# Kernel tuning notes

Hardware: AMD Instinct MI355X
Metric: run time of the kernel (lower is better)

The kernel has to match this reference:

```python
import jax, jax.numpy as jnp
import numpy as np

N_NODES = 100000
N_EDGES = 3200000
IN_CH, HID_CH, OUT_CH = 128, 64, 40


def gcn_conv(x, row, col, norm, W, b, n_nodes):
    # linear transform first (PyG GCNConv order), then normalized aggregation
    h = x @ W                                   # [N, out]
    msg = h[row] * norm[:, None]                # [E+N, out] gathered & scaled
    out = jax.ops.segment_sum(msg, col, num_segments=n_nodes)
    return out + b


def setup_inputs() -> dict:
    key = jax.random.key(0)
    k0, k1, k2, k3, k4, k5 = jax.random.split(key, 6)
    x = jax.random.normal(k0, (N_NODES, IN_CH), dtype=jnp.float32)
    edge_index = jax.random.randint(k1, (2, N_EDGES), 0, N_NODES, dtype=jnp.int64)
    # Glorot-ish init for weights
    W1 = jax.random.normal(k2, (IN_CH, HID_CH), dtype=jnp.float32) * (1.0 / np.sqrt(IN_CH))
    b1 = jnp.zeros((HID_CH,), dtype=jnp.float32)
    W2 = jax.random.normal(k3, (HID_CH, OUT_CH), dtype=jnp.float32) * (1.0 / np.sqrt(HID_CH))
    b2 = jnp.zeros((OUT_CH,), dtype=jnp.float32)
    return {"x": x, "edge_index": edge_index, "original_size": N_NODES,
            "W1": W1, "b1": b1, "W2": W2, "b2": b2}


def reference(x, edge_index, original_size, W1, b1, W2, b2):
    n = x.shape[0]
    # add self-loops (GCNConv default)
    loops = jnp.arange(n, dtype=edge_index.dtype)
    row = jnp.concatenate([edge_index[0], loops])   # source
    col = jnp.concatenate([edge_index[1], loops])   # target
    # symmetric normalization: deg over targets with unit edge weights
    deg = jax.ops.segment_sum(jnp.ones_like(col, dtype=x.dtype), col, num_segments=n)
    dinv = jnp.where(deg > 0, jax.lax.rsqrt(deg), 0.0)
    norm = dinv[row] * dinv[col]                    # [E+N]
    h = gcn_conv(x, row, col, norm, W1, b1, n)
    h = gcn_conv(h, row, col, norm, W2, b2, n)
    out = jax.nn.log_softmax(h, axis=1)
    return out[:original_size]
```

## Files before the change

### kernel.cpp

```cpp
#include <hip/hip_runtime.h>
#include <math.h>


#define NN 100000
#define NE 3200000
#define NBUK 391
#define BCAP 8704
#define EPB 16384


__global__ void k_zero(int* __restrict__ p, int n) {
  int i = blockIdx.x * blockDim.x + threadIdx.x;
  if (i < n) p[i] = 0;
}


__device__ __forceinline__ unsigned bf16rne(float x) {
  unsigned u = __float_as_uint(x);
  return (u + 0x7fffu + ((u >> 16) & 1u)) >> 16;
}
__device__ __forceinline__ unsigned pack2(float lo, float hi) {
  return bf16rne(lo) | (bf16rne(hi) << 16);
}


__global__ __launch_bounds__(256) void k_bucket(const int* __restrict__ ei,
                                                int* __restrict__ tail,
                                                unsigned* __restrict__ bucket) {
  __shared__ int hist[NBUK], wbase[NBUK], loc[NBUK];
  const int tid = threadIdx.x;
  const int beg = blockIdx.x * EPB;
  const int end = min(beg + EPB, NE);
  const int* col = ei + NE;
  for (int b = tid; b < NBUK; b += 256) { hist[b] = 0; loc[b] = 0; }
  __syncthreads();
  for (int e = beg + tid * 4; e < end; e += 1024) {
    int4 c4 = *(const int4*)(col + e);
    atomicAdd(&hist[c4.x >> 8], 1);
    atomicAdd(&hist[c4.y >> 8], 1);
    atomicAdd(&hist[c4.z >> 8], 1);
    atomicAdd(&hist[c4.w >> 8], 1);
  }
  __syncthreads();
  for (int b = tid; b < NBUK; b += 256)
    wbase[b] = atomicAdd(&tail[b], hist[b]);
  __syncthreads();
  for (int e = beg + tid * 4; e < end; e += 1024) {
    int4 c4 = *(const int4*)(col + e);
    int4 r4 = *(const int4*)(ei + e);
    {
      int b = c4.x >> 8;
      unsigned pos = (unsigned)(wbase[b] + atomicAdd(&loc[b], 1));
      if (pos < BCAP) bucket[(size_t)b * BCAP + pos] = ((unsigned)r4.x << 8) | (unsigned)(c4.x & 255);
    }
    {
      int b = c4.y >> 8;
      unsigned pos = (unsigned)(wbase[b] + atomicAdd(&loc[b], 1));
      if (pos < BCAP) bucket[(size_t)b * BCAP + pos] = ((unsigned)r4.y << 8) | (unsigned)(c4.y & 255);
    }
    {
      int b = c4.z >> 8;
      unsigned pos = (unsigned)(wbase[b] + atomicAdd(&loc[b], 1));
      if (pos < BCAP) bucket[(size_t)b * BCAP + pos] = ((unsigned)r4.z << 8) | (unsigned)(c4.z & 255);
    }
    {
      int b = c4.w >> 8;
      unsigned pos = (unsigned)(wbase[b] + atomicAdd(&loc[b], 1));
      if (pos < BCAP) bucket[(size_t)b * BCAP + pos] = ((unsigned)r4.w << 8) | (unsigned)(c4.w & 255);
    }
  }
}


__global__ void k_bstart(const int* __restrict__ tail, int* __restrict__ bstart) {
  const int tid = threadIdx.x, lane = tid & 63, wid = tid >> 6;
  int v = (tid < NBUK) ? min(tail[tid], BCAP) : 0;
  int s = v;
  #pragma unroll
  for (int d = 1; d < 64; d <<= 1) { int t = __shfl_up(s, d, 64); if (lane >= d) s += t; }
  __shared__ int wsum[8];
  if (lane == 63) wsum[wid] = s;
  __syncthreads();
  int wpre = 0;
  for (int w = 0; w < wid; ++w) wpre += wsum[w];
  int excl = wpre + s - v;
  if (tid <= NBUK) bstart[tid] = excl;
}


__global__ __launch_bounds__(256) void k_sort(const unsigned* __restrict__ bucket,
                                              const int* __restrict__ tail,
                                              const int* __restrict__ bstart,
                                              int* __restrict__ csr_src,
                                              int* __restrict__ offsets,
                                              float* __restrict__ dinv) {
  __shared__ int h[256], base_[256], loc[256];
  __shared__ int sorted[BCAP];
  __shared__ int wsum[4];
  const int b = blockIdx.x;
  const int lo = b << 8;
  const int nc = min(256, NN - lo);
  const int n = min(tail[b], BCAP);
  const int seg0 = bstart[b];
  const unsigned* __restrict__ bk = bucket + (size_t)b * BCAP;
  const int tid = threadIdx.x, lane = tid & 63, wid = tid >> 6;
  h[tid] = 0; loc[tid] = 0;
  __syncthreads();
  int i = tid * 4;
  for (; i + 3 < n; i += 1024) {
    uint4 v = *(const uint4*)(bk + i);
    atomicAdd(&h[v.x & 255u], 1);
    atomicAdd(&h[v.y & 255u], 1);
    atomicAdd(&h[v.z & 255u], 1);
    atomicAdd(&h[v.w & 255u], 1);
  }
  for (; i < n; ++i) atomicAdd(&h[bk[i] & 255u], 1);
  __syncthreads();
  {
    int v = h[tid];
    int s = v;
    #pragma unroll
    for (int d = 1; d < 64; d <<= 1) { int t = __shfl_up(s, d, 64); if (lane >= d) s += t; }
    if (lane == 63) wsum[wid] = s;
    __syncthreads();
    int wpre = 0;
    #pragma unroll
    for (int w = 0; w < 4; ++w) if (w < wid) wpre += wsum[w];
    int excl = wpre + s - v;
    base_[tid] = excl;
    if (tid < nc) {
      dinv[lo + tid] = rsqrtf((float)(v + 1));
      offsets[lo + tid] = seg0 + excl;
    }
  }
  if (b == 0 && tid == 0) offsets[NN] = bstart[NBUK];
  __syncthreads();
  i = tid * 4;
  for (; i + 3 < n; i += 1024) {
    uint4 v = *(const uint4*)(bk + i);
    { int c = v.x & 255u; sorted[base_[c] + atomicAdd(&loc[c], 1)] = (int)(v.x >> 8); }
    { int c = v.y & 255u; sorted[base_[c] + atomicAdd(&loc[c], 1)] = (int)(v.y >> 8); }
    { int c = v.z & 255u; sorted[base_[c] + atomicAdd(&loc[c], 1)] = (int)(v.z >> 8); }
    { int c = v.w & 255u; sorted[base_[c] + atomicAdd(&loc[c], 1)] = (int)(v.w >> 8); }
  }
  for (; i < n; ++i) {
    unsigned ent = bk[i];
    int c = ent & 255u;
    sorted[base_[c] + atomicAdd(&loc[c], 1)] = (int)(ent >> 8);
  }
  __syncthreads();
  for (int t = tid; t < n; t += 256) csr_src[seg0 + t] = sorted[t];
}


__global__ __launch_bounds__(256) void k_gemm1(const float* __restrict__ x,
                                               const float* __restrict__ W1,
                                               const float* __restrict__ dinv,
                                               unsigned* __restrict__ m1b) {
  __shared__ float ws[128 * 64];
  __shared__ float xt[16 * 132];
  const int tid = threadIdx.x;
  const int row0 = blockIdx.x * 128;
  {
    const float4* __restrict__ w4 = (const float4*)W1;
    float4* __restrict__ s4 = (float4*)ws;
    for (int i = tid; i < 128 * 16; i += 256) s4[i] = w4[i];
  }
  const int cg = tid & 7;
  const int rg = tid >> 3;
  const int srow = tid & 127;
  const int skh = tid >> 7;
  float acc[4][8];
  #pragma unroll
  for (int i = 0; i < 4; ++i)
    #pragma unroll
    for (int j = 0; j < 8; ++j) acc[i][j] = 0.f;
  const float4* __restrict__ xt4 = (const float4*)xt;
  const float4* __restrict__ ws4 = (const float4*)ws;
  for (int ks = 0; ks < 8; ++ks) {
    __syncthreads();
    {
      int grow = row0 + srow; if (grow > NN - 1) grow = NN - 1;
      const float* xp = x + (size_t)grow * 128 + ks * 16 + skh * 8;
      float4 va = *(const float4*)xp;
      float4 vb = *(const float4*)(xp + 4);
      const int kb = skh * 8;
      xt[(kb + 0) * 132 + srow] = va.x;
      xt[(kb + 1) * 132 + srow] = va.y;
      xt[(kb + 2) * 132 + srow] = va.z;
      xt[(kb + 3) * 132 + srow] = va.w;
      xt[(kb + 4) * 132 + srow] = vb.x;
      xt[(kb + 5) * 132 + srow] = vb.y;
      xt[(kb + 6) * 132 + srow] = vb.z;
      xt[(kb + 7) * 132 + srow] = vb.w;
    }
    __syncthreads();
    #pragma unroll 4
    for (int kk = 0; kk < 16; ++kk) {
      const int k = ks * 16 + kk;
      float4 xv = xt4[kk * 33 + rg];
      float4 wa = ws4[k * 16 + cg * 2];
      float4 wb = ws4[k * 16 + cg * 2 + 1];
      float xr[4] = {xv.x, xv.y, xv.z, xv.w};
      float wc[8] = {wa.x, wa.y, wa.z, wa.w, wb.x, wb.y, wb.z, wb.w};
      #pragma unroll
      for (int i = 0; i < 4; ++i)
        #pragma unroll
        for (int j = 0; j < 8; ++j)
          acc[i][j] = fmaf(xr[i], wc[j], acc[i][j]);
    }
  }
  #pragma unroll
  for (int i = 0; i < 4; ++i) {
    const int row = row0 + rg * 4 + i;
    if (row < NN) {
      const float d = dinv[row];
      uint4 o;
      o.x = pack2(acc[i][0] * d, acc[i][1] * d);
      o.y = pack2(acc[i][2] * d, acc[i][3] * d);
      o.z = pack2(acc[i][4] * d, acc[i][5] * d);
      o.w = pack2(acc[i][6] * d, acc[i][7] * d);
      ((uint4*)m1b)[row * 8 + cg] = o;
    }
  }
}


#define ACC8(v, f)                                                   \
  acc[0] = fmaf(__uint_as_float((v).x << 16), (f), acc[0]);          \
  acc[1] = fmaf(__uint_as_float((v).x & 0xffff0000u), (f), acc[1]);  \
  acc[2] = fmaf(__uint_as_float((v).y << 16), (f), acc[2]);          \
  acc[3] = fmaf(__uint_as_float((v).y & 0xffff0000u), (f), acc[3]);  \
  acc[4] = fmaf(__uint_as_float((v).z << 16), (f), acc[4]);          \
  acc[5] = fmaf(__uint_as_float((v).z & 0xffff0000u), (f), acc[5]);  \
  acc[6] = fmaf(__uint_as_float((v).w << 16), (f), acc[6]);          \
  acc[7] = fmaf(__uint_as_float((v).w & 0xffff0000u), (f), acc[7]);


__global__ __launch_bounds__(256) void k_agg1(const unsigned* __restrict__ m1b,
                                              const int* __restrict__ offsets,
                                              const int* __restrict__ csr_src,
                                              const float* __restrict__ dinv,
                                              const float* __restrict__ b1,
                                              float* __restrict__ a1) {
  const int node = blockIdx.x * 4 + (threadIdx.x >> 6);
  const int lane = threadIdx.x & 63;
  const int e = lane >> 3;
  const int q = lane & 7;
  const uint4* __restrict__ m1v = (const uint4*)m1b;
  const int beg = offsets[node], end = offsets[node + 1];
  float acc[8];
  #pragma unroll
  for (int j = 0; j < 8; ++j) acc[j] = 0.f;
  for (int p = beg; p < end; p += 32) {
    const int i0 = p + e, i1 = p + 8 + e, i2 = p + 16 + e, i3 = p + 24 + e;
    const int s0 = csr_src[i0 < end ? i0 : beg];
    const int s1 = csr_src[i1 < end ? i1 : beg];
    const int s2 = csr_src[i2 < end ? i2 : beg];
    const int s3 = csr_src[i3 < end ? i3 : beg];
    const float f0 = (i0 < end) ? 1.f : 0.f;
    const float f1 = (i1 < end) ? 1.f : 0.f;
    const float f2 = (i2 < end) ? 1.f : 0.f;
    const float f3 = (i3 < end) ? 1.f : 0.f;
    uint4 v0 = m1v[s0 * 8 + q];
    uint4 v1 = m1v[s1 * 8 + q];
    uint4 v2 = m1v[s2 * 8 + q];
    uint4 v3 = m1v[s3 * 8 + q];
    ACC8(v0, f0);
    ACC8(v1, f1);
    ACC8(v2, f2);
    ACC8(v3, f3);
  }
  #pragma unroll
  for (int j = 0; j < 8; ++j) {
    acc[j] += __shfl_xor(acc[j], 8, 64);
    acc[j] += __shfl_xor(acc[j], 16, 64);
    acc[j] += __shfl_xor(acc[j], 32, 64);
  }
  if (e == 0) {
    uint4 sv = m1v[node * 8 + q];
    const float d = dinv[node];
    float4 bb0 = ((const float4*)b1)[q * 2];
    float4 bb1 = ((const float4*)b1)[q * 2 + 1];
    float4 o0, o1;
    o0.x = (acc[0] + __uint_as_float(sv.x << 16)) * d + bb0.x;
    o0.y = (acc[1] + __uint_as_float(sv.x & 0xffff0000u)) * d + bb0.y;
    o0.z = (acc[2] + __uint_as_float(sv.y << 16)) * d + bb0.z;
    o0.w = (acc[3] + __uint_as_float(sv.y & 0xffff0000u)) * d + bb0.w;
    o1.x = (acc[4] + __uint_as_float(sv.z << 16)) * d + bb1.x;
    o1.y = (acc[5] + __uint_as_float(sv.z & 0xffff0000u)) * d + bb1.y;
    o1.z = (acc[6] + __uint_as_float(sv.w << 16)) * d + bb1.z;
    o1.w = (acc[7] + __uint_as_float(sv.w & 0xffff0000u)) * d + bb1.w;
    ((float4*)a1)[node * 16 + q * 2] = o0;
    ((float4*)a1)[node * 16 + q * 2 + 1] = o1;
  }
}


__global__ __launch_bounds__(256) void k_gemm2(const float* __restrict__ a1,
                                               const float* __restrict__ W2,
                                               const float* __restrict__ dinv,
                                               unsigned* __restrict__ m2b) {
  __shared__ float ws[64 * 40];
  const int tid = threadIdx.x;
  for (int k = tid; k < 64 * 40; k += 256) ws[k] = W2[k];
  __syncthreads();
  const int idx = blockIdx.x * 256 + tid;
  if (idx >= NN * 20) return;
  const int node = idx / 20;
  const int c0 = (idx - node * 20) * 2;
  const float4* __restrict__ a4 = (const float4*)(a1 + node * 64);
  float acc0 = 0.f, acc1 = 0.f;
  #pragma unroll
  for (int k4 = 0; k4 < 16; ++k4) {
    float4 a = a4[k4];
    acc0 = fmaf(a.x, ws[(k4 * 4 + 0) * 40 + c0], acc0);
    acc1 = fmaf(a.x, ws[(k4 * 4 + 0) * 40 + c0 + 1], acc1);
    acc0 = fmaf(a.y, ws[(k4 * 4 + 1) * 40 + c0], acc0);
    acc1 = fmaf(a.y, ws[(k4 * 4 + 1) * 40 + c0 + 1], acc1);
    acc0 = fmaf(a.z, ws[(k4 * 4 + 2) * 40 + c0], acc0);
    acc1 = fmaf(a.z, ws[(k4 * 4 + 2) * 40 + c0 + 1], acc1);
    acc0 = fmaf(a.w, ws[(k4 * 4 + 3) * 40 + c0], acc0);
    acc1 = fmaf(a.w, ws[(k4 * 4 + 3) * 40 + c0 + 1], acc1);
  }
  const float d = dinv[node];
  m2b[idx] = pack2(acc0 * d, acc1 * d);
}


__device__ __forceinline__ float shfl1(float v, int src) {
  return __shfl(v, src & 63, 64);
}

__global__ __launch_bounds__(256) void k_agg2(const unsigned* __restrict__ m2b,
                                              const int* __restrict__ offsets,
                                              const int* __restrict__ csr_src,
                                              const float* __restrict__ dinv,
                                              const float* __restrict__ b2,
                                              float* __restrict__ out) {
  const int node = blockIdx.x * 4 + (threadIdx.x >> 6);
  const int lane = threadIdx.x & 63;
  const bool act = lane < 60;
  const int e = act ? (lane / 5) : 0;
  const int q = act ? (lane - e * 5) : 0;
  const uint4* __restrict__ m2v = (const uint4*)m2b;
  const int beg = offsets[node], end = offsets[node + 1];
  float acc[8];
  #pragma unroll
  for (int j = 0; j < 8; ++j) acc[j] = 0.f;
  for (int p = beg; p < end; p += 48) {
    const int i0 = p + e, i1 = p + 12 + e, i2 = p + 24 + e, i3 = p + 36 + e;
    const int s0 = csr_src[i0 < end ? i0 : beg];
    const int s1 = csr_src[i1 < end ? i1 : beg];
    const int s2 = csr_src[i2 < end ? i2 : beg];
    const int s3 = csr_src[i3 < end ? i3 : beg];
    const float f0 = (act && i0 < end) ? 1.f : 0.f;
    const float f1 = (act && i1 < end) ? 1.f : 0.f;
    const float f2 = (act && i2 < end) ? 1.f : 0.f;
    const float f3 = (act && i3 < end) ? 1.f : 0.f;
    uint4 v0 = m2v[s0 * 5 + q];
    uint4 v1 = m2v[s1 * 5 + q];
    uint4 v2 = m2v[s2 * 5 + q];
    uint4 v3 = m2v[s3 * 5 + q];
    ACC8(v0, f0);
    ACC8(v1, f1);
    ACC8(v2, f2);
    ACC8(v3, f3);
  }
  #pragma unroll
  for (int j = 0; j < 8; ++j) acc[j] += shfl1(acc[j], lane + 30);
  #pragma unroll
  for (int j = 0; j < 8; ++j) acc[j] += shfl1(acc[j], lane + 15);
  #pragma unroll
  for (int j = 0; j < 8; ++j) {
    float t1 = shfl1(acc[j], lane + 5);
    float t2 = shfl1(acc[j], lane + 10);
    acc[j] += t1 + t2;
  }
  const bool lead = (lane < 5);
  float r[8];
  #pragma unroll
  for (int j = 0; j < 8; ++j) r[j] = 0.f;
  if (lead) {
    uint4 sv = m2v[node * 5 + lane];
    const float d = dinv[node];
    float4 bb0 = ((const float4*)b2)[lane * 2];
    float4 bb1 = ((const float4*)b2)[lane * 2 + 1];
    r[0] = (acc[0] + __uint_as_float(sv.x << 16)) * d + bb0.x;
    r[1] = (acc[1] + __uint_as_float(sv.x & 0xffff0000u)) * d + bb0.y;
    r[2] = (acc[2] + __uint_as_float(sv.y << 16)) * d + bb0.z;
    r[3] = (acc[3] + __uint_as_float(sv.y & 0xffff0000u)) * d + bb0.w;
    r[4] = (acc[4] + __uint_as_float(sv.z << 16)) * d + bb1.x;
    r[5] = (acc[5] + __uint_as_float(sv.z & 0xffff0000u)) * d + bb1.y;
    r[6] = (acc[6] + __uint_as_float(sv.w << 16)) * d + bb1.z;
    r[7] = (acc[7] + __uint_as_float(sv.w & 0xffff0000u)) * d + bb1.w;
  }
  float mx = -INFINITY;
  if (lead) {
    mx = fmaxf(fmaxf(fmaxf(r[0], r[1]), fmaxf(r[2], r[3])),
               fmaxf(fmaxf(r[4], r[5]), fmaxf(r[6], r[7])));
  }
  #pragma unroll
  for (int d = 4; d > 0; d >>= 1) mx = fmaxf(mx, __shfl_xor(mx, d, 8));
  float se = 0.f;
  if (lead) {
    se = __expf(r[0] - mx) + __expf(r[1] - mx) + __expf(r[2] - mx) +
         __expf(r[3] - mx) + __expf(r[4] - mx) + __expf(r[5] - mx) +
         __expf(r[6] - mx) + __expf(r[7] - mx);
  }
  #pragma unroll
  for (int d = 4; d > 0; d >>= 1) se += __shfl_xor(se, d, 8);
  if (lead) {
    const float lse = mx + logf(se);
    float4 o0, o1;
    o0.x = r[0] - lse; o0.y = r[1] - lse; o0.z = r[2] - lse; o0.w = r[3] - lse;
    o1.x = r[4] - lse; o1.y = r[5] - lse; o1.z = r[6] - lse; o1.w = r[7] - lse;
    ((float4*)out)[node * 10 + lane * 2] = o0;
    ((float4*)out)[node * 10 + lane * 2 + 1] = o1;
  }
}


extern "C" void kernel_launch(void* const* d_in, const int* in_sizes, int n_in,
                              void* d_out, int out_size, void* d_ws, size_t ws_size,
                              hipStream_t stream) {
  const float* x   = (const float*)d_in[0];
  const int*   ei  = (const int*)d_in[1];
  const float* W1  = (const float*)d_in[3];
  const float* b1  = (const float*)d_in[4];
  const float* W2  = (const float*)d_in[5];
  const float* b2  = (const float*)d_in[6];
  float*       out = (float*)d_out;

  char* ws = (char*)d_ws;
  int*      tail    = (int*)(ws + 0);
  int*      bstart  = (int*)(ws + (size_t)4 * 1024);
  int*      offsets = (int*)(ws + (size_t)8 * 1024);
  float*    dinv    = (float*)(ws + (size_t)512 * 1024);
  int*      csr_src = (int*)(ws + (size_t)1024 * 1024);
  unsigned* bucket  = (unsigned*)(ws + (size_t)14 * 1024 * 1024);
  unsigned* m1b     = (unsigned*)(ws + (size_t)14 * 1024 * 1024);
  float*    a1      = (float*)(ws + (size_t)40 * 1024 * 1024);
  unsigned* m2b     = m1b;

  k_zero<<<2, 256, 0, stream>>>(tail, NBUK);
  k_bucket<<<(NE + EPB - 1) / EPB, 256, 0, stream>>>(ei, tail, bucket);
  k_bstart<<<1, 512, 0, stream>>>(tail, bstart);
  k_sort<<<NBUK, 256, 0, stream>>>(bucket, tail, bstart, csr_src, offsets, dinv);
  k_gemm1<<<(NN + 127) / 128, 256, 0, stream>>>(x, W1, dinv, m1b);
  k_agg1<<<NN / 4, 256, 0, stream>>>(m1b, offsets, csr_src, dinv, b1, a1);
  k_gemm2<<<(NN * 20 + 255) / 256, 256, 0, stream>>>(a1, W2, dinv, m2b);
  k_agg2<<<NN / 4, 256, 0, stream>>>(m2b, offsets, csr_src, dinv, b2, out);
}
```

Before: 221.3 us.

## Fuse edge bucketing with first GEMM via global degree-count pre-pass

Adds a separate atomic degree-count kernel so the first GEMM can compute dinv directly from column counts, removing its dependency on the sort. That lets the bucketing and GEMM1 work share a single launch, with different block ranges doing different jobs so they overlap. The zero kernel is replaced by memset calls and the workspace layout is reshuffled so the bucket and m1b buffers no longer alias. The cost is an extra pass over the column indices with 3.2M global atomics, plus a larger shared-memory footprint for the bucketing blocks, which may reduce occupancy.

```diff
diff --git a/kernel.cpp b/kernel.cpp
--- a/kernel.cpp
+++ b/kernel.cpp
@@ -7,12 +7,8 @@
 #define NBUK 391
 #define BCAP 8704
 #define EPB 16384
-
-
-__global__ void k_zero(int* __restrict__ p, int n) {
-  int i = blockIdx.x * blockDim.x + threadIdx.x;
-  if (i < n) p[i] = 0;
-}
+#define NBB ((NE + EPB - 1) / EPB)
+#define NGB 782
 
 
 __device__ __forceinline__ unsigned bf16rne(float x) {
@@ -24,49 +20,138 @@
 }
 
 
-__global__ __launch_bounds__(256) void k_bucket(const int* __restrict__ ei,
-                                                int* __restrict__ tail,
-                                                unsigned* __restrict__ bucket) {
-  __shared__ int hist[NBUK], wbase[NBUK], loc[NBUK];
+__global__ __launch_bounds__(256) void k_deg(const int* __restrict__ ei,
+                                             int* __restrict__ colcnt) {
+  const int i = blockIdx.x * 256 + threadIdx.x;
+  const int4 c4 = *(const int4*)(ei + NE + (size_t)i * 4);
+  atomicAdd(&colcnt[c4.x], 1);
+  atomicAdd(&colcnt[c4.y], 1);
+  atomicAdd(&colcnt[c4.z], 1);
+  atomicAdd(&colcnt[c4.w], 1);
+}
+
+
+__global__ __launch_bounds__(256) void k_bucket_gemm1(const int* __restrict__ ei,
+                                                      int* __restrict__ tail,
+                                                      unsigned* __restrict__ bucket,
+                                                      const float* __restrict__ x,
+                                                      const float* __restrict__ W1,
+                                                      const int* __restrict__ colcnt,
+                                                      unsigned* __restrict__ m1b) {
+  __shared__ float smem[128 * 64 + 16 * 132];
   const int tid = threadIdx.x;
-  const int beg = blockIdx.x * EPB;
-  const int end = min(beg + EPB, NE);
-  const int* col = ei + NE;
-  for (int b = tid; b < NBUK; b += 256) { hist[b] = 0; loc[b] = 0; }
-  __syncthreads();
-  for (int e = beg + tid * 4; e < end; e += 1024) {
-    int4 c4 = *(const int4*)(col + e);
-    atomicAdd(&hist[c4.x >> 8], 1);
-    atomicAdd(&hist[c4.y >> 8], 1);
-    atomicAdd(&hist[c4.z >> 8], 1);
-    atomicAdd(&hist[c4.w >> 8], 1);
-  }
-  __syncthreads();
-  for (int b = tid; b < NBUK; b += 256)
-    wbase[b] = atomicAdd(&tail[b], hist[b]);
-  __syncthreads();
-  for (int e = beg + tid * 4; e < end; e += 1024) {
-    int4 c4 = *(const int4*)(col + e);
-    int4 r4 = *(const int4*)(ei + e);
+  const int bx = blockIdx.x;
+
+  if (bx < NBB) {
+    int* hist  = (int*)smem;
+    int* wbase = hist + NBUK;
+    int* loc   = wbase + NBUK;
+    const int beg = bx * EPB;
+    const int end = min(beg + EPB, NE);
+    const int* col = ei + NE;
+    for (int b = tid; b < NBUK; b += 256) { hist[b] = 0; loc[b] = 0; }
+    __syncthreads();
+    for (int e = beg + tid * 4; e < end; e += 1024) {
+      int4 c4 = *(const int4*)(col + e);
+      atomicAdd(&hist[c4.x >> 8], 1);
+      atomicAdd(&hist[c4.y >> 8], 1);
+      atomicAdd(&hist[c4.z >> 8], 1);
+      atomicAdd(&hist[c4.w >> 8], 1);
+    }
+    __syncthreads();
+    for (int b = tid; b < NBUK; b += 256)
+      wbase[b] = atomicAdd(&tail[b], hist[b]);
+    __syncthreads();
+    for (int e = beg + tid * 4; e < end; e += 1024) {
+      int4 c4 = *(const int4*)(col + e);
+      int4 r4 = *(const int4*)(ei + e);
+      {
+        int b = c4.x >> 8;
+        unsigned pos = (unsigned)(wbase[b] + atomicAdd(&loc[b], 1));
+        if (pos < BCAP) bucket[(size_t)b * BCAP + pos] = ((unsigned)r4.x << 8) | (unsigned)(c4.x & 255);
+      }
+      {
+        int b = c4.y >> 8;
+        unsigned pos = (unsigned)(wbase[b] + atomicAdd(&loc[b], 1));
+        if (pos < BCAP) bucket[(size_t)b * BCAP + pos] = ((unsigned)r4.y << 8) | (unsigned)(c4.y & 255);
+      }
+      {
+        int b = c4.z >> 8;
+        unsigned pos = (unsigned)(wbase[b] + atomicAdd(&loc[b], 1));
+        if (pos < BCAP) bucket[(size_t)b * BCAP + pos] = ((unsigned)r4.z << 8) | (unsigned)(c4.z & 255);
+      }
+      {
+        int b = c4.w >> 8;
+        unsigned pos = (unsigned)(wbase[b] + atomicAdd(&loc[b], 1));
+        if (pos < BCAP) bucket[(size_t)b * BCAP + pos] = ((unsigned)r4.w << 8) | (unsigned)(c4.w & 255);
+      }
+    }
+    return;
+  }
+
+  float* ws = smem;
+  float* xt = smem + 128 * 64;
+  const int row0 = (bx - NBB) * 128;
+  {
+    const float4* __restrict__ w4 = (const float4*)W1;
+    float4* __restrict__ s4 = (float4*)ws;
+    for (int i = tid; i < 128 * 16; i += 256) s4[i] = w4[i];
+  }
+  const int cg = tid & 7;
+  const int rg = tid >> 3;
+  const int srow = tid & 127;
+  const int skh = tid >> 7;
+  float acc[4][8];
+  #pragma unroll
+  for (int i = 0; i < 4; ++i)
+    #pragma unroll
+    for (int j = 0; j < 8; ++j) acc[i][j] = 0.f;
+  const float4* __restrict__ xt4 = (const float4*)xt;
+  const float4* __restrict__ ws4 = (const float4*)ws;
+  for (int ks = 0; ks < 8; ++ks) {
+    __syncthreads();
     {
-      int b = c4.x >> 8;
-      unsigned pos = (unsigned)(wbase[b] + atomicAdd(&loc[b], 1));
-      if (pos < BCAP) bucket[(size_t)b * BCAP + pos] = ((unsigned)r4.x << 8) | (unsigned)(c4.x & 255);
-    }
-    {
-      int b = c4.y >> 8;
-      unsigned pos = (unsigned)(wbase[b] + atomicAdd(&loc[b], 1));
-      if (pos < BCAP) bucket[(size_t)b * BCAP + pos] = ((unsigned)r4.y << 8) | (unsigned)(c4.y & 255);
-    }
-    {
-      int b = c4.z >> 8;
-      unsigned pos = (unsigned)(wbase[b] + atomicAdd(&loc[b], 1));
-      if (pos < BCAP) bucket[(size_t)b * BCAP + pos] = ((unsigned)r4.z << 8) | (unsigned)(c4.z & 255);
-    }
-    {
-      int b = c4.w >> 8;
-      unsigned pos = (unsigned)(wbase[b] + atomicAdd(&loc[b], 1));
-      if (pos < BCAP) bucket[(size_t)b * BCAP + pos] = ((unsigned)r4.w << 8) | (unsigned)(c4.w & 255);
+      int grow = row0 + srow; if (grow > NN - 1) grow = NN - 1;
+      const float* xp = x + (size_t)grow * 128 + ks * 16 + skh * 8;
+      float4 va = *(const float4*)xp;
+      float4 vb = *(const float4*)(xp + 4);
+      const int kb = skh * 8;
+      xt[(kb + 0) * 132 + srow] = va.x;
+      xt[(kb + 1) * 132 + srow] = va.y;
+      xt[(kb + 2) * 132 + srow] = va.z;
+      xt[(kb + 3) * 132 + srow] = va.w;
+      xt[(kb + 4) * 132 + srow] = vb.x;
+      xt[(kb + 5) * 132 + srow] = vb.y;
+      xt[(kb + 6) * 132 + srow] = vb.z;
+      xt[(kb + 7) * 132 + srow] = vb.w;
+    }
+    __syncthreads();
+    #pragma unroll 4
+    for (int kk = 0; kk < 16; ++kk) {
+      const int k = ks * 16 + kk;
+      float4 xv = xt4[kk * 33 + rg];
+      float4 wa = ws4[k * 16 + cg * 2];
+      float4 wb = ws4[k * 16 + cg * 2 + 1];
+      float xr[4] = {xv.x, xv.y, xv.z, xv.w};
+      float wc[8] = {wa.x, wa.y, wa.z, wa.w, wb.x, wb.y, wb.z, wb.w};
+      #pragma unroll
+      for (int i = 0; i < 4; ++i)
+        #pragma unroll
+        for (int j = 0; j < 8; ++j)
+          acc[i][j] = fmaf(xr[i], wc[j], acc[i][j]);
+    }
+  }
+  #pragma unroll
+  for (int i = 0; i < 4; ++i) {
+    const int row = row0 + rg * 4 + i;
+    if (row < NN) {
+      const float d = rsqrtf((float)(colcnt[row] + 1));
+      uint4 o;
+      o.x = pack2(acc[i][0] * d, acc[i][1] * d);
+      o.y = pack2(acc[i][2] * d, acc[i][3] * d);
+      o.z = pack2(acc[i][4] * d, acc[i][5] * d);
+      o.w = pack2(acc[i][6] * d, acc[i][7] * d);
+      ((uint4*)m1b)[row * 8 + cg] = o;
     }
   }
 }
@@ -150,79 +235,6 @@
   }
   __syncthreads();
   for (int t = tid; t < n; t += 256) csr_src[seg0 + t] = sorted[t];
-}
-
-
-__global__ __launch_bounds__(256) void k_gemm1(const float* __restrict__ x,
-                                               const float* __restrict__ W1,
-                                               const float* __restrict__ dinv,
-                                               unsigned* __restrict__ m1b) {
-  __shared__ float ws[128 * 64];
-  __shared__ float xt[16 * 132];
-  const int tid = threadIdx.x;
-  const int row0 = blockIdx.x * 128;
-  {
-    const float4* __restrict__ w4 = (const float4*)W1;
-    float4* __restrict__ s4 = (float4*)ws;
-    for (int i = tid; i < 128 * 16; i += 256) s4[i] = w4[i];
-  }
-  const int cg = tid & 7;
-  const int rg = tid >> 3;
-  const int srow = tid & 127;
-  const int skh = tid >> 7;
-  float acc[4][8];
-  #pragma unroll
-  for (int i = 0; i < 4; ++i)
-    #pragma unroll
-    for (int j = 0; j < 8; ++j) acc[i][j] = 0.f;
-  const float4* __restrict__ xt4 = (const float4*)xt;
-  const float4* __restrict__ ws4 = (const float4*)ws;
-  for (int ks = 0; ks < 8; ++ks) {
-    __syncthreads();
-    {
-      int grow = row0 + srow; if (grow > NN - 1) grow = NN - 1;
-      const float* xp = x + (size_t)grow * 128 + ks * 16 + skh * 8;
-      float4 va = *(const float4*)xp;
-      float4 vb = *(const float4*)(xp + 4);
-      const int kb = skh * 8;
-      xt[(kb + 0) * 132 + srow] = va.x;
-      xt[(kb + 1) * 132 + srow] = va.y;
-      xt[(kb + 2) * 132 + srow] = va.z;
-      xt[(kb + 3) * 132 + srow] = va.w;
-      xt[(kb + 4) * 132 + srow] = vb.x;
-      xt[(kb + 5) * 132 + srow] = vb.y;
-      xt[(kb + 6) * 132 + srow] = vb.z;
-      xt[(kb + 7) * 132 + srow] = vb.w;
-    }
-    __syncthreads();
-    #pragma unroll 4
-    for (int kk = 0; kk < 16; ++kk) {
-      const int k = ks * 16 + kk;
-      float4 xv = xt4[kk * 33 + rg];
-      float4 wa = ws4[k * 16 + cg * 2];
-      float4 wb = ws4[k * 16 + cg * 2 + 1];
-      float xr[4] = {xv.x, xv.y, xv.z, xv.w};
-      float wc[8] = {wa.x, wa.y, wa.z, wa.w, wb.x, wb.y, wb.z, wb.w};
-      #pragma unroll
-      for (int i = 0; i < 4; ++i)
-        #pragma unroll
-        for (int j = 0; j < 8; ++j)
-          acc[i][j] = fmaf(xr[i], wc[j], acc[i][j]);
-    }
-  }
-  #pragma unroll
-  for (int i = 0; i < 4; ++i) {
-    const int row = row0 + rg * 4 + i;
-    if (row < NN) {
-      const float d = dinv[row];
-      uint4 o;
-      o.x = pack2(acc[i][0] * d, acc[i][1] * d);
-      o.y = pack2(acc[i][2] * d, acc[i][3] * d);
-      o.z = pack2(acc[i][4] * d, acc[i][5] * d);
-      o.w = pack2(acc[i][6] * d, acc[i][7] * d);
-      ((uint4*)m1b)[row * 8 + cg] = o;
-    }
-  }
 }
 
 
@@ -437,17 +449,19 @@
   int*      bstart  = (int*)(ws + (size_t)4 * 1024);
   int*      offsets = (int*)(ws + (size_t)8 * 1024);
   float*    dinv    = (float*)(ws + (size_t)512 * 1024);
-  int*      csr_src = (int*)(ws + (size_t)1024 * 1024);
-  unsigned* bucket  = (unsigned*)(ws + (size_t)14 * 1024 * 1024);
-  unsigned* m1b     = (unsigned*)(ws + (size_t)14 * 1024 * 1024);
-  float*    a1      = (float*)(ws + (size_t)40 * 1024 * 1024);
+  int*      colcnt  = (int*)(ws + (size_t)1024 * 1024);
+  int*      csr_src = (int*)(ws + (size_t)1536 * 1024);
+  unsigned* m1b     = (unsigned*)(ws + (size_t)14848 * 1024);
+  unsigned* bucket  = (unsigned*)(ws + (size_t)28160 * 1024);
+  float*    a1      = (float*)(ws + (size_t)28160 * 1024);
   unsigned* m2b     = m1b;
 
-  k_zero<<<2, 256, 0, stream>>>(tail, NBUK);
-  k_bucket<<<(NE + EPB - 1) / EPB, 256, 0, stream>>>(ei, tail, bucket);
+  hipMemsetAsync(tail, 0, NBUK * 4, stream);
+  hipMemsetAsync(colcnt, 0, NN * 4, stream);
+  k_deg<<<NE / 1024, 256, 0, stream>>>(ei, colcnt);
+  k_bucket_gemm1<<<NBB + NGB, 256, 0, stream>>>(ei, tail, bucket, x, W1, colcnt, m1b);
   k_bstart<<<1, 512, 0, stream>>>(tail, bstart);
   k_sort<<<NBUK, 256, 0, stream>>>(bucket, tail, bstart, csr_src, offsets, dinv);
-  k_gemm1<<<(NN + 127) / 128, 256, 0, stream>>>(x, W1, dinv, m1b);
   k_agg1<<<NN / 4, 256, 0, stream>>>(m1b, offsets, csr_src, dinv, b1, a1);
   k_gemm2<<<(NN * 20 + 255) / 256, 256, 0, stream>>>(a1, W2, dinv, m2b);
   k_agg2<<<NN / 4, 256, 0, stream>>>(m2b, offsets, csr_src, dinv, b2, out);
```

After: 333.4 us. 50.6% more time.
